# Kernel tuning notes

Measured on AMD Instinct MI355X. Metric: run time of the kernel, lower is better.

Reference implementation:

```python
import jax, jax.numpy as jnp
import numpy as np

B, T, C = 4, 2048, 1024
H = 16
HD = C // H


def setup_inputs() -> dict:
    key = jax.random.key(0)
    k1, k2, k3 = jax.random.split(key, 3)
    x = jax.random.normal(k1, (B, T, C), dtype=jnp.float32)
    w_qkv = jax.random.normal(k2, (C, 3 * C), dtype=jnp.float32) * (C ** -0.5)
    w_proj = jax.random.normal(k3, (C, C), dtype=jnp.float32) * (C ** -0.5)
    b_proj = jnp.zeros((C,), dtype=jnp.float32)
    return {"x": x, "w_qkv": w_qkv, "w_proj": w_proj, "b_proj": b_proj}


def reference(x, w_qkv, w_proj, b_proj):
    Bd, Td, Cd = x.shape
    scale = HD ** -0.5
    qkv = x @ w_qkv  # [B,T,3C]
    q, k, v = jnp.split(qkv, 3, axis=-1)
    # [B,H,T,HD]
    q = q.reshape(Bd, Td, H, HD).transpose(0, 2, 1, 3)
    k = k.reshape(Bd, Td, H, HD).transpose(0, 2, 1, 3)
    v = v.reshape(Bd, Td, H, HD).transpose(0, 2, 1, 3)
    att = jnp.einsum('bhqd,bhkd->bhqk', q, k) * scale
    causal = jnp.triu(jnp.ones((Td, Td), dtype=bool), k=1)
    att = jnp.where(causal, -jnp.inf, att)
    att = jax.nn.softmax(att, axis=-1)
    y = jnp.einsum('bhqk,bhkd->bhqd', att, v)
    y = y.transpose(0, 2, 1, 3).reshape(Bd, Td, Cd)
    return y @ w_proj + b_proj
```

## Files before the change

kernel.cpp:

```cpp
#include <hip/hip_runtime.h>

typedef unsigned short u16;
typedef __attribute__((ext_vector_type(8))) short short8;
typedef __attribute__((ext_vector_type(4))) short short4v;
typedef __attribute__((ext_vector_type(4))) float floatx4;
typedef __attribute__((ext_vector_type(4))) unsigned short ushort4v;

#define B_ 4
#define T_ 2048
#define C_ 1024
#define H_ 16
#define HD_ 64

static __device__ __forceinline__ u16 f2bf(float f) {
  union { float f; unsigned int i; } c; c.f = f;
  unsigned int u = c.i;
  return (u16)((u + 0x7FFFu + ((u >> 16) & 1u)) >> 16);
}
static __device__ __forceinline__ u16 truncbf(float f) {
  union { float f; unsigned int i; } c; c.f = f;
  return (u16)(c.i >> 16);
}

static __device__ __forceinline__ void gload16(const u16* g, u16* l) {
  __builtin_amdgcn_global_load_lds(
      (const __attribute__((address_space(1))) unsigned int*)(g),
      (__attribute__((address_space(3))) unsigned int*)(l), 16, 0, 0);
}

__global__ __launch_bounds__(256) void prep_k(const float* __restrict__ x,
                                              const float* __restrict__ w_qkv,
                                              const float* __restrict__ w_proj,
                                              u16* __restrict__ xbf,
                                              u16* __restrict__ wqkvT,
                                              u16* __restrict__ wprojT) {
  const int bid = blockIdx.x;
  if (bid < 8192) {
    const int i = bid * 256 + threadIdx.x;
    const float4 f = ((const float4*)x)[i];
    ushort4v o;
    o.x = f2bf(f.x); o.y = f2bf(f.y); o.z = f2bf(f.z); o.w = f2bf(f.w);
    *(ushort4v*)(xbf + (size_t)i * 4) = o;
    return;
  }
  __shared__ u16 tile[32][33];
  const float* in;
  u16* out;
  int R, Cc, tb;
  if (bid < 11264) {
    in = w_qkv; out = wqkvT; R = C_; Cc = 3 * C_; tb = bid - 8192;
  } else {
    in = w_proj; out = wprojT; R = C_; Cc = C_; tb = bid - 11264;
  }
  const int tpr = Cc / 32;
  const int bx = (tb % tpr) * 32;
  const int by = (tb / tpr) * 32;
  const int tx = threadIdx.x & 31;
  const int ty = threadIdx.x >> 5;
  #pragma unroll
  for (int i = ty; i < 32; i += 8)
    tile[i][tx] = f2bf(in[(size_t)(by + i) * Cc + bx + tx]);
  __syncthreads();
  #pragma unroll
  for (int i = ty; i < 32; i += 8)
    out[(size_t)(bx + i) * R + by + tx] = tile[tx][i];
}

__global__ __launch_bounds__(256) void vtrans_k(const u16* __restrict__ qkv,
                                                u16* __restrict__ vt) {
  __shared__ u16 tile[64][74];
  const int tt = blockIdx.x;
  const int bh = blockIdx.y;
  const int b = bh >> 4, h = bh & 15;
  const int tid = threadIdx.x;
  const u16* src = qkv + ((size_t)b * T_ + tt * 64) * (3 * C_) + 2 * C_ + h * HD_;
  #pragma unroll
  for (int ss = tid; ss < 512; ss += 256) {
    const int row = ss >> 3, c8 = (ss & 7) * 8;
    *(short8*)(&tile[row][c8]) = *(const short8*)(src + (size_t)row * (3 * C_) + c8);
  }
  __syncthreads();
  u16* dst = vt + (size_t)bh * HD_ * T_ + tt * 64;
  #pragma unroll
  for (int ss = tid; ss < 512; ss += 256) {
    const int tc = (ss & 7) * 8, d = ss >> 3;
    short8 o;
    #pragma unroll
    for (int j = 0; j < 8; j++) o[j] = (short)tile[tc + j][d];
    *(short8*)(dst + (size_t)d * T_ + tc) = o;
  }
}

template <int MODE>
__global__ __launch_bounds__(256) void gemm_bt(const u16* __restrict__ A,
                                               const u16* __restrict__ Bt,
                                               u16* __restrict__ outb,
                                               float* __restrict__ outf,
                                               const float* __restrict__ bias,
                                               int M, int N, int K) {
  __shared__ __align__(16) u16 As[2][128 * 32];
  __shared__ __align__(16) u16 Bs[2][128 * 32];
  const int tN = blockIdx.x * 128;
  const int tM = blockIdx.y * 128;
  const int tid = threadIdx.x;
  const int wave = tid >> 6;
  const int lane = tid & 63;
  const int lr = lane & 15;
  const int quad = lane >> 4;
  const int wm = (wave >> 1) * 64;
  const int wn = (wave & 1) * 64;

  const int srow = lane >> 2;
  const int skofs = ((lane & 3) ^ ((lane >> 3) & 3)) * 8;

  const floatx4 zf = {0.f, 0.f, 0.f, 0.f};
  floatx4 acc[4][4];
  #pragma unroll
  for (int i = 0; i < 4; i++)
    #pragma unroll
    for (int j = 0; j < 4; j++) acc[i][j] = zf;

  const int csw = (lr >> 1) & 3;

  for (int k0 = 0; k0 < K; k0 += 64) {
    __syncthreads();
    #pragma unroll
    for (int half = 0; half < 2; half++) {
      const int kk = k0 + half * 32;
      #pragma unroll
      for (int j = 0; j < 2; j++) {
        const int seg = wave * 2 + j;
        const int row = seg * 16 + srow;
        gload16(A + (size_t)(tM + row) * K + kk + skofs, &As[half][seg * 512]);
        gload16(Bt + (size_t)(tN + row) * K + kk + skofs, &Bs[half][seg * 512]);
      }
    }
    __syncthreads();

    #pragma unroll
    for (int half = 0; half < 2; half++) {
      short8 af[4], bfr[4];
      #pragma unroll
      for (int mt = 0; mt < 4; mt++)
        af[mt] = *(const short8*)(&As[half][(wm + mt * 16 + lr) * 32 + ((quad ^ csw) * 8)]);
      #pragma unroll
      for (int nt = 0; nt < 4; nt++)
        bfr[nt] = *(const short8*)(&Bs[half][(wn + nt * 16 + lr) * 32 + ((quad ^ csw) * 8)]);
      #pragma unroll
      for (int mt = 0; mt < 4; mt++)
        #pragma unroll
        for (int nt = 0; nt < 4; nt++)
          acc[mt][nt] = __builtin_amdgcn_mfma_f32_16x16x32_bf16(af[mt], bfr[nt],
                                                                acc[mt][nt], 0, 0, 0);
    }
  }

  #pragma unroll
  for (int mt = 0; mt < 4; mt++) {
    const int m0 = tM + wm + mt * 16 + quad * 4;
    #pragma unroll
    for (int nt = 0; nt < 4; nt++) {
      const int n = tN + wn + nt * 16 + lr;
      #pragma unroll
      for (int r = 0; r < 4; r++) {
        const float v = acc[mt][nt][r];
        const size_t m = (size_t)(m0 + r);
        if (MODE == 2) outf[m * N + n] = v + bias[n];
        else           outb[m * N + n] = f2bf(v);
      }
    }
  }
}

__global__ __launch_bounds__(256, 4) void attn_k(const u16* __restrict__ qkv,
                                                 const u16* __restrict__ vt,
                                                 u16* __restrict__ y) {
  __shared__ __align__(16) u16 Ks[64 * 64];
  __shared__ __align__(16) u16 Vs[64 * 64];
  const int bid = blockIdx.x;
  const int s = bid >> 3;
  const int qp = s >> 3;
  const int bh = ((s & 7) << 3) | (bid & 7);
  const int b = bh >> 4, h = bh & 15;
  const int tid = threadIdx.x;
  const int wave = tid >> 6;
  const int lane = tid & 63;
  const int lr = lane & 15;
  const int quad = lane >> 4;
  const int qtA = qp, qtB = 31 - qp;

  const int srow = lane >> 3;
  const int skofs = ((lane & 7) ^ ((lane >> 3) & 7)) * 8;
  const int gsw = lr & 7;

  const size_t RS = 3 * C_;
  const u16* qcol = qkv + (size_t)b * T_ * RS + h * HD_;
  const u16* kcol = qcol + C_;

  const size_t qrA = (size_t)(qtA * 64 + wave * 16 + lr) * RS;
  const size_t qrB = (size_t)(qtB * 64 + wave * 16 + lr) * RS;
  const short8 aq0A = *(const short8*)(qcol + qrA + quad * 8);
  const short8 aq1A = *(const short8*)(qcol + qrA + 32 + quad * 8);
  const short8 aq0B = *(const short8*)(qcol + qrB + quad * 8);
  const short8 aq1B = *(const short8*)(qcol + qrB + 32 + quad * 8);

  const floatx4 zf = {0.f, 0.f, 0.f, 0.f};
  const float C1 = 0.125f * 1.44269504f;
  const float C2 = -16.0f * 1.44269504f;

  floatx4 accA[4], accB[4];
  #pragma unroll
  for (int i = 0; i < 4; i++) { accA[i] = zf; accB[i] = zf; }
  float psumA = 0.f, psumB = 0.f;

  for (int kt = 0; kt <= qtB; kt++) {
    const bool doA = (kt <= qtA);
    const bool diagA = (kt == qtA), diagB = (kt == qtB);
    __syncthreads();
    #pragma unroll
    for (int j = 0; j < 2; j++) {
      const int seg = wave * 2 + j;
      const int row = seg * 8 + srow;
      gload16(kcol + (size_t)(kt * 64 + row) * RS + skofs, &Ks[seg * 512]);
      gload16(vt + ((size_t)bh * HD_ + row) * T_ + kt * 64 + skofs, &Vs[seg * 512]);
    }
    __syncthreads();

    float peA[4][4], peB[4][4];
    #pragma unroll
    for (int nt = 0; nt < 4; nt++) {
      const short8 bk0 =
          *(const short8*)(&Ks[(nt * 16 + lr) * 64 + ((quad ^ gsw) * 8)]);
      const short8 bk1 =
          *(const short8*)(&Ks[(nt * 16 + lr) * 64 + (((quad + 4) ^ gsw) * 8)]);
      {
        floatx4 st = __builtin_amdgcn_mfma_f32_16x16x32_bf16(
            bk1, aq1B,
            __builtin_amdgcn_mfma_f32_16x16x32_bf16(bk0, aq0B, zf, 0, 0, 0),
            0, 0, 0);
        #pragma unroll
        for (int r = 0; r < 4; r++) {
          float pe = __builtin_amdgcn_exp2f(fmaf(st[r], C1, C2));
          if (diagB && (nt * 16 + quad * 4 + r > wave * 16 + lr)) pe = 0.f;
          peB[nt][r] = pe;
          psumB += pe;
        }
      }
      if (doA) {
        floatx4 st = __builtin_amdgcn_mfma_f32_16x16x32_bf16(
            bk1, aq1A,
            __builtin_amdgcn_mfma_f32_16x16x32_bf16(bk0, aq0A, zf, 0, 0, 0),
            0, 0, 0);
        #pragma unroll
        for (int r = 0; r < 4; r++) {
          float pe = __builtin_amdgcn_exp2f(fmaf(st[r], C1, C2));
          if (diagA && (nt * 16 + quad * 4 + r > wave * 16 + lr)) pe = 0.f;
          peA[nt][r] = pe;
          psumA += pe;
        }
      }
    }

    short8 pB[2], pA[2];
    #pragma unroll
    for (int h2 = 0; h2 < 2; h2++) {
      #pragma unroll
      for (int j = 0; j < 8; j++) {
        pB[h2][j] = (short)truncbf(peB[2 * h2 + (j >> 2)][j & 3]);
        if (doA) pA[h2][j] = (short)truncbf(peA[2 * h2 + (j >> 2)][j & 3]);
      }
    }

    #pragma unroll
    for (int h2 = 0; h2 < 2; h2++) {
      #pragma unroll
      for (int dt = 0; dt < 4; dt++) {
        const int base = (dt * 16 + lr) * 64;
        const int cl = h2 * 4 + (quad >> 1);
        const int off_lo = ((cl ^ gsw) * 8) + (quad & 1) * 4;
        const int off_hi = (((cl + 2) ^ gsw) * 8) + (quad & 1) * 4;
        const short4v vlo = *(const short4v*)(&Vs[base + off_lo]);
        const short4v vhi = *(const short4v*)(&Vs[base + off_hi]);
        const short8 av = __builtin_shufflevector(vlo, vhi, 0, 1, 2, 3, 4, 5, 6, 7);
        accB[dt] = __builtin_amdgcn_mfma_f32_16x16x32_bf16(av, pB[h2], accB[dt], 0, 0, 0);
        if (doA)
          accA[dt] = __builtin_amdgcn_mfma_f32_16x16x32_bf16(av, pA[h2], accA[dt], 0, 0, 0);
      }
    }
  }

  #pragma unroll
  for (int ph = 0; ph < 2; ph++) {
    const int qt = ph ? qtB : qtA;
    const floatx4* acc = ph ? accB : accA;
    float ssum = ph ? psumB : psumA;
    ssum += __shfl_xor(ssum, 16, 64);
    ssum += __shfl_xor(ssum, 32, 64);
    const float inv = 1.f / ssum;
    const int qg = qt * 64 + wave * 16 + lr;
    u16* yrow = y + ((size_t)(b * T_ + qg)) * C_ + h * HD_;
    #pragma unroll
    for (int dt = 0; dt < 4; dt++) {
      ushort4v o;
      #pragma unroll
      for (int r = 0; r < 4; r++) o[r] = f2bf(acc[dt][r] * inv);
      *(ushort4v*)(yrow + dt * 16 + quad * 4) = o;
    }
  }
}

extern "C" void kernel_launch(void* const* d_in, const int* in_sizes, int n_in,
                              void* d_out, int out_size, void* d_ws, size_t ws_size,
                              hipStream_t stream) {
  const float* x      = (const float*)d_in[0];
  const float* w_qkv  = (const float*)d_in[1];
  const float* w_proj = (const float*)d_in[2];
  const float* b_proj = (const float*)d_in[3];
  float* out = (float*)d_out;

  u16* ws = (u16*)d_ws;
  const size_t SZ = (size_t)B_ * T_ * C_;
  u16* xbf    = ws;
  u16* wqkvT  = xbf + SZ;
  u16* wprojT = wqkvT + (size_t)3 * C_ * C_;
  u16* qkvw   = wprojT + (size_t)C_ * C_;
  u16* vtw    = qkvw + 3 * SZ;
  u16* yw     = xbf;

  prep_k<<<12288, 256, 0, stream>>>(x, w_qkv, w_proj, xbf, wqkvT, wprojT);
  gemm_bt<1><<<dim3(3 * C_ / 128, B_ * T_ / 128), 256, 0, stream>>>(
      xbf, wqkvT, qkvw, nullptr, nullptr, B_ * T_, 3 * C_, C_);
  vtrans_k<<<dim3(T_ / 64, B_ * H_), 256, 0, stream>>>(qkvw, vtw);
  attn_k<<<1024, 256, 0, stream>>>(qkvw, vtw, yw);
  gemm_bt<2><<<dim3(C_ / 128, B_ * T_ / 128), 256, 0, stream>>>(
      yw, wprojT, nullptr, out, b_proj, B_ * T_, C_, C_);
}
```

Before: 244.3 us.

## Remap GEMM tiles, compute softmax sums via MFMA, pack bf16 with perm

The GEMM kernels now use a 1D grid remapped so that consecutive blocks share N tiles across groups of M tiles, aiming at better L2 reuse. The projection output is written with nontemporal stores. In attention, the per-lane softmax denominator sums and the cross-lane shuffles are replaced by an extra MFMA against a ones vector, and the bf16 packing uses v_perm on pairs. Together these aim to cut VALU work and cache pollution, at the cost of extra MFMA issue slots. The denominator now sums the bf16-truncated probabilities instead of the fp32 ones.

```diff
diff --git a/kernel.cpp b/kernel.cpp
--- a/kernel.cpp
+++ b/kernel.cpp
@@ -17,9 +17,9 @@
   unsigned int u = c.i;
   return (u16)((u + 0x7FFFu + ((u >> 16) & 1u)) >> 16);
 }
-static __device__ __forceinline__ u16 truncbf(float f) {
-  union { float f; unsigned int i; } c; c.f = f;
-  return (u16)(c.i >> 16);
+static __device__ __forceinline__ unsigned pk2(float lo, float hi) {
+  union { float f; unsigned u; } a, b; a.f = hi; b.f = lo;
+  return __builtin_amdgcn_perm(a.u, b.u, 0x07060302u);
 }
 
 static __device__ __forceinline__ void gload16(const u16* g, u16* l) {
@@ -100,8 +100,10 @@
                                                int M, int N, int K) {
   __shared__ __align__(16) u16 As[2][128 * 32];
   __shared__ __align__(16) u16 Bs[2][128 * 32];
-  const int tN = blockIdx.x * 128;
-  const int tM = blockIdx.y * 128;
+  const int bid = blockIdx.x;
+  const int s = bid >> 3;
+  const int tM = ((bid & 7) * 8 + (s & 7)) * 128;
+  const int tN = (s >> 3) * 128;
   const int tid = threadIdx.x;
   const int wave = tid >> 6;
   const int lane = tid & 63;
@@ -165,7 +167,7 @@
       for (int r = 0; r < 4; r++) {
         const float v = acc[mt][nt][r];
         const size_t m = (size_t)(m0 + r);
-        if (MODE == 2) outf[m * N + n] = v + bias[n];
+        if (MODE == 2) __builtin_nontemporal_store(v + bias[n], &outf[m * N + n]);
         else           outb[m * N + n] = f2bf(v);
       }
     }
@@ -207,11 +209,12 @@
   const floatx4 zf = {0.f, 0.f, 0.f, 0.f};
   const float C1 = 0.125f * 1.44269504f;
   const float C2 = -16.0f * 1.44269504f;
+  const short8 vones = {16256, 16256, 16256, 16256, 16256, 16256, 16256, 16256};
 
   floatx4 accA[4], accB[4];
+  floatx4 accSA = zf, accSB = zf;
   #pragma unroll
   for (int i = 0; i < 4; i++) { accA[i] = zf; accB[i] = zf; }
-  float psumA = 0.f, psumB = 0.f;
 
   for (int kt = 0; kt <= qtB; kt++) {
     const bool doA = (kt <= qtA);
@@ -243,7 +246,6 @@
           float pe = __builtin_amdgcn_exp2f(fmaf(st[r], C1, C2));
           if (diagB && (nt * 16 + quad * 4 + r > wave * 16 + lr)) pe = 0.f;
           peB[nt][r] = pe;
-          psumB += pe;
         }
       }
       if (doA) {
@@ -256,7 +258,6 @@
           float pe = __builtin_amdgcn_exp2f(fmaf(st[r], C1, C2));
           if (diagA && (nt * 16 + quad * 4 + r > wave * 16 + lr)) pe = 0.f;
           peA[nt][r] = pe;
-          psumA += pe;
         }
       }
     }
@@ -264,15 +265,30 @@
     short8 pB[2], pA[2];
     #pragma unroll
     for (int h2 = 0; h2 < 2; h2++) {
-      #pragma unroll
-      for (int j = 0; j < 8; j++) {
-        pB[h2][j] = (short)truncbf(peB[2 * h2 + (j >> 2)][j & 3]);
-        if (doA) pA[h2][j] = (short)truncbf(peA[2 * h2 + (j >> 2)][j & 3]);
+      union { unsigned u[4]; short8 s8; } w;
+      w.u[0] = pk2(peB[2 * h2][0], peB[2 * h2][1]);
+      w.u[1] = pk2(peB[2 * h2][2], peB[2 * h2][3]);
+      w.u[2] = pk2(peB[2 * h2 + 1][0], peB[2 * h2 + 1][1]);
+      w.u[3] = pk2(peB[2 * h2 + 1][2], peB[2 * h2 + 1][3]);
+      pB[h2] = w.s8;
+    }
+    if (doA) {
+      #pragma unroll
+      for (int h2 = 0; h2 < 2; h2++) {
+        union { unsigned u[4]; short8 s8; } w;
+        w.u[0] = pk2(peA[2 * h2][0], peA[2 * h2][1]);
+        w.u[1] = pk2(peA[2 * h2][2], peA[2 * h2][3]);
+        w.u[2] = pk2(peA[2 * h2 + 1][0], peA[2 * h2 + 1][1]);
+        w.u[3] = pk2(peA[2 * h2 + 1][2], peA[2 * h2 + 1][3]);
+        pA[h2] = w.s8;
       }
     }
 
     #pragma unroll
     for (int h2 = 0; h2 < 2; h2++) {
+      accSB = __builtin_amdgcn_mfma_f32_16x16x32_bf16(vones, pB[h2], accSB, 0, 0, 0);
+      if (doA)
+        accSA = __builtin_amdgcn_mfma_f32_16x16x32_bf16(vones, pA[h2], accSA, 0, 0, 0);
       #pragma unroll
       for (int dt = 0; dt < 4; dt++) {
         const int base = (dt * 16 + lr) * 64;
@@ -293,10 +309,7 @@
   for (int ph = 0; ph < 2; ph++) {
     const int qt = ph ? qtB : qtA;
     const floatx4* acc = ph ? accB : accA;
-    float ssum = ph ? psumB : psumA;
-    ssum += __shfl_xor(ssum, 16, 64);
-    ssum += __shfl_xor(ssum, 32, 64);
-    const float inv = 1.f / ssum;
+    const float inv = 1.f / (ph ? accSB[0] : accSA[0]);
     const int qg = qt * 64 + wave * 16 + lr;
     u16* yrow = y + ((size_t)(b * T_ + qg)) * C_ + h * HD_;
     #pragma unroll
@@ -328,10 +341,10 @@
   u16* yw     = xbf;
 
   prep_k<<<12288, 256, 0, stream>>>(x, w_qkv, w_proj, xbf, wqkvT, wprojT);
-  gemm_bt<1><<<dim3(3 * C_ / 128, B_ * T_ / 128), 256, 0, stream>>>(
+  gemm_bt<1><<<1536, 256, 0, stream>>>(
       xbf, wqkvT, qkvw, nullptr, nullptr, B_ * T_, 3 * C_, C_);
   vtrans_k<<<dim3(T_ / 64, B_ * H_), 256, 0, stream>>>(qkvw, vtw);
   attn_k<<<1024, 256, 0, stream>>>(qkvw, vtw, yw);
-  gemm_bt<2><<<dim3(C_ / 128, B_ * T_ / 128), 256, 0, stream>>>(
+  gemm_bt<2><<<512, 256, 0, stream>>>(
       yw, wprojT, nullptr, out, b_proj, B_ * T_, C_, C_);
 }
```

After: 246.0 us. No clear change (+0.7%).
